# Kernel optimization log

Measured on AMD Instinct MI355X. Metric: run time of the kernel, lower is better.

## Reference

```python
import jax, jax.numpy as jnp
import numpy as np

N_NODES = 50000
N_EDGES = 1600000
IN_FEATS = 512
N_HIDDEN = 128
N_CLASSES = 40


def setup_inputs() -> dict:
    key = jax.random.key(0)
    k1, k2, k3, k4, k5, k6, k7 = jax.random.split(key, 7)
    features = jax.random.normal(k1, (N_NODES, IN_FEATS), dtype=jnp.float32)
    src = jax.random.randint(k2, (N_EDGES,), 0, N_NODES)
    dst = jax.random.randint(k3, (N_EDGES,), 0, N_NODES)
    # Glorot-ish init for weights, zeros for biases (DGL GraphConv defaults)
    W1 = jax.random.normal(k4, (IN_FEATS, N_HIDDEN), dtype=jnp.float32) / np.sqrt(IN_FEATS)
    b1 = jnp.zeros((N_HIDDEN,), dtype=jnp.float32)
    W2 = jax.random.normal(k5, (N_HIDDEN, N_CLASSES), dtype=jnp.float32) / np.sqrt(N_HIDDEN)
    b2 = jnp.zeros((N_CLASSES,), dtype=jnp.float32)
    return {"features": features, "W1": W1, "b1": b1, "W2": W2, "b2": b2,
            "src": src, "dst": dst}


def _norms(src, dst, n_nodes):
    ones = jnp.ones(src.shape[0], dtype=jnp.float32)
    deg_out = jax.ops.segment_sum(ones, src, num_segments=n_nodes)
    deg_in = jax.ops.segment_sum(ones, dst, num_segments=n_nodes)
    # clamp degree >= 1 as DGL does
    norm_src = jax.lax.rsqrt(jnp.maximum(deg_out, 1.0))
    norm_dst = jax.lax.rsqrt(jnp.maximum(deg_in, 1.0))
    return norm_src, norm_dst


def _graph_conv(x, W, b, src, dst, norm_src, norm_dst, n_nodes):
    # DGL GraphConv with norm='both'; in_feats > out_feats so W applied first
    h = x @ W                                   # [N, out]
    h = h * norm_src[:, None]                   # src-side D^{-1/2}
    msgs = h[src]                               # gather [E, out]
    agg = jax.ops.segment_sum(msgs, dst, num_segments=n_nodes)  # scatter-add
    agg = agg * norm_dst[:, None]               # dst-side D^{-1/2}
    return agg + b


def reference(features, W1, b1, W2, b2, src, dst):
    norm_src, norm_dst = _norms(src, dst, N_NODES)
    h = _graph_conv(features, W1, b1, src, dst, norm_src, norm_dst, N_NODES)
    h = jax.nn.relu(h)
    # dropout is identity at inference
    h = _graph_conv(h, W2, b2, src, dst, norm_src, norm_dst, N_NODES)
    return h
```

## Files before the change

kernel.cpp:

```cpp
#include <hip/hip_runtime.h>
#include <hip/hip_bf16.h>

#define N_NODES 50000
#define N_EDGES 1600000
#define IN_FEATS 512
#define N_HIDDEN 128
#define N_CLASSES 40
#define NBKT 782
#define NBLK 800
#define EPB 2000
#define NROWPAD 50048

typedef __attribute__((ext_vector_type(8))) short bf16x8;
typedef __attribute__((ext_vector_type(4))) float f32x4;

__device__ __forceinline__ unsigned short f2bf(float f) {
    unsigned u = __float_as_uint(f);
    u = (u + 0x7FFFu + ((u >> 16) & 1u)) >> 16;
    return (unsigned short)u;
}
__device__ __forceinline__ float bf2f(unsigned short h) {
    return __uint_as_float(((unsigned)h) << 16);
}
__device__ __forceinline__ unsigned pk_bf(float a, float b) {
    __hip_bfloat162 h = __float22bfloat162_rn(make_float2(a, b));
    union { __hip_bfloat162 v; unsigned u; } c;
    c.v = h;
    return c.u;
}

__device__ __forceinline__ void cvt8(float4 a, float4 b, bf16x8& h, bf16x8& l) {
    unsigned h0 = pk_bf(a.x, a.y), h1 = pk_bf(a.z, a.w);
    unsigned h2 = pk_bf(b.x, b.y), h3 = pk_bf(b.z, b.w);
    unsigned l0 = pk_bf(a.x - __uint_as_float(h0 << 16),
                        a.y - __uint_as_float(h0 & 0xffff0000u));
    unsigned l1 = pk_bf(a.z - __uint_as_float(h1 << 16),
                        a.w - __uint_as_float(h1 & 0xffff0000u));
    unsigned l2 = pk_bf(b.x - __uint_as_float(h2 << 16),
                        b.y - __uint_as_float(h2 & 0xffff0000u));
    unsigned l3 = pk_bf(b.z - __uint_as_float(h3 << 16),
                        b.w - __uint_as_float(h3 & 0xffff0000u));
    union U { unsigned u[4]; bf16x8 v; };
    U H; H.u[0] = h0; H.u[1] = h1; H.u[2] = h2; H.u[3] = h3; h = H.v;
    U L; L.u[0] = l0; L.u[1] = l1; L.u[2] = l2; L.u[3] = l3; l = L.v;
}

__global__ __launch_bounds__(256) void setup_cvt(
    const float* __restrict__ W1, const float* __restrict__ W2,
    unsigned short* __restrict__ W1ch, unsigned short* __restrict__ W1cl,
    unsigned short* __restrict__ W2th, unsigned short* __restrict__ W2tl) {
    int i = blockIdx.x * 256 + threadIdx.x;
    if (i < IN_FEATS * N_HIDDEN) {
        int k = i >> 7, c = i & 127;
        float v = W1[i];
        unsigned short h = f2bf(v);
        int o = (k >> 5) * 4096 + c * 32 + (k & 31);
        W1ch[o] = h;
        W1cl[o] = f2bf(v - bf2f(h));
    } else {
        int j = i - IN_FEATS * N_HIDDEN;
        int n = j >> 7, k = j & 127;
        float v = (n < N_CLASSES) ? W2[k * N_CLASSES + n] : 0.f;
        unsigned short h = f2bf(v);
        W2th[n * 128 + k] = h;
        W2tl[n * 128 + k] = f2bf(v - bf2f(h));
    }
}


#define MFJ(AH, AL, BH, BL, ACC)                                              \
    ACC = __builtin_amdgcn_mfma_f32_16x16x32_bf16(AH, BH, ACC, 0, 0, 0);      \
    ACC = __builtin_amdgcn_mfma_f32_16x16x32_bf16(AH, BL, ACC, 0, 0, 0);      \
    ACC = __builtin_amdgcn_mfma_f32_16x16x32_bf16(AL, BH, ACC, 0, 0, 0);

#define LOADB(KC)                                                             \
    const bf16x8 bh0 = *(const bf16x8*)(wbh + (KC) * 4096);                   \
    const bf16x8 bh1 = *(const bf16x8*)(wbh + (KC) * 4096 + 512);             \
    const bf16x8 bl0 = *(const bf16x8*)(wbl + (KC) * 4096);                   \
    const bf16x8 bl1 = *(const bf16x8*)(wbl + (KC) * 4096 + 512);

#define CORE()                                                                \
    bf16x8 ah0, al0, ah1, al1, ah2, al2, ah3, al3;                            \
    cvt8(xa00, xa01, ah0, al0); cvt8(xa10, xa11, ah1, al1);                   \
    cvt8(xa20, xa21, ah2, al2); cvt8(xa30, xa31, ah3, al3);                   \
    MFJ(ah0, al0, bh0, bl0, acc[0][0]) MFJ(ah0, al0, bh1, bl1, acc[0][1])     \
    MFJ(ah1, al1, bh0, bl0, acc[1][0]) MFJ(ah1, al1, bh1, bl1, acc[1][1])     \
    MFJ(ah2, al2, bh0, bl0, acc[2][0]) MFJ(ah2, al2, bh1, bl1, acc[2][1])     \
    MFJ(ah3, al3, bh0, bl0, acc[3][0]) MFJ(ah3, al3, bh1, bl1, acc[3][1])

__device__ __forceinline__ int imin(int a, int b) { return a < b ? a : b; }

__global__ __launch_bounds__(256) void megaA(
    const int* __restrict__ src, const int* __restrict__ dst,
    int* __restrict__ histD, int* __restrict__ histS,
    const float* __restrict__ X, const unsigned short* __restrict__ Wch,
    const unsigned short* __restrict__ Wcl, unsigned short* __restrict__ Hb) {
    __shared__ int hd[NBKT], hs[NBKT];
    const int tid = threadIdx.x;

    if (blockIdx.x >= NBKT) {
        int b = blockIdx.x - NBKT;
        for (int i = tid; i < NBKT; i += 256) { hd[i] = 0; hs[i] = 0; }
        __syncthreads();
        int e0 = b * EPB;
        for (int i = tid; i < EPB; i += 256) {
            atomicAdd(&hd[dst[e0 + i] >> 6], 1);
            atomicAdd(&hs[src[e0 + i] >> 6], 1);
        }
        __syncthreads();
        for (int i = tid; i < NBKT; i += 256) {
            histD[b * NBKT + i] = hd[i];
            histS[b * NBKT + i] = hs[i];
        }
        return;
    }
    const int lane = tid & 63;
    const int wv = tid >> 6;
    const int m = lane & 15;
    const int q = lane >> 4;
    const int q8 = q * 8;
    const int row0 = blockIdx.x * 64;

    const unsigned short* wbh = Wch + (wv * 32 + m) * 32 + q8;
    const unsigned short* wbl = Wcl + (wv * 32 + m) * 32 + q8;

    const float* xr0 = &X[(size_t)imin(row0 + m,      N_NODES - 1) * IN_FEATS + q8];
    const float* xr1 = &X[(size_t)imin(row0 + 16 + m, N_NODES - 1) * IN_FEATS + q8];
    const float* xr2 = &X[(size_t)imin(row0 + 32 + m, N_NODES - 1) * IN_FEATS + q8];
    const float* xr3 = &X[(size_t)imin(row0 + 48 + m, N_NODES - 1) * IN_FEATS + q8];

    f32x4 acc[4][2];
#pragma unroll
    for (int i = 0; i < 4; i++)
#pragma unroll
        for (int j = 0; j < 2; j++) acc[i][j] = (f32x4){0.f, 0.f, 0.f, 0.f};

    float4 xa00 = *(const float4*)(xr0),     xa01 = *(const float4*)(xr0 + 4);
    float4 xa10 = *(const float4*)(xr1),     xa11 = *(const float4*)(xr1 + 4);
    float4 xa20 = *(const float4*)(xr2),     xa21 = *(const float4*)(xr2 + 4);
    float4 xa30 = *(const float4*)(xr3),     xa31 = *(const float4*)(xr3 + 4);

    for (int kc = 0; kc < 15; kc++) {
        LOADB(kc)
        const int o = (kc + 1) * 32;
        float4 xn00 = *(const float4*)(xr0 + o), xn01 = *(const float4*)(xr0 + o + 4);
        float4 xn10 = *(const float4*)(xr1 + o), xn11 = *(const float4*)(xr1 + o + 4);
        float4 xn20 = *(const float4*)(xr2 + o), xn21 = *(const float4*)(xr2 + o + 4);
        float4 xn30 = *(const float4*)(xr3 + o), xn31 = *(const float4*)(xr3 + o + 4);
        CORE()
        xa00 = xn00; xa01 = xn01; xa10 = xn10; xa11 = xn11;
        xa20 = xn20; xa21 = xn21; xa30 = xn30; xa31 = xn31;
    }
    {
        LOADB(15)
        CORE()
    }

#pragma unroll
    for (int i = 0; i < 4; i++) {
#pragma unroll
        for (int r = 0; r < 4; r++) {
            int grow = row0 + i * 16 + q * 4 + r;
            if (grow < N_NODES) {
#pragma unroll
                for (int j = 0; j < 2; j++)
                    Hb[(size_t)grow * N_HIDDEN + wv * 32 + j * 16 + m] = f2bf(acc[i][j][r]);
            }
        }
    }
}

__global__ __launch_bounds__(256) void p2_local(
    const int* __restrict__ histD, const int* __restrict__ histS,
    int* __restrict__ baseD, int* __restrict__ baseS,
    int* __restrict__ totD, int* __restrict__ totS) {
    int wv = threadIdx.x >> 6, lane = threadIdx.x & 63;
    int w = blockIdx.x * 4 + wv;
    if (w >= NBKT) return;
    int runD = 0, runS = 0;
#pragma unroll
    for (int c = 0; c < 13; c++) {
        int blk = c * 64 + lane;
        int vD = 0, vS = 0;
        if (blk < NBLK) {
            vD = histD[blk * NBKT + w];
            vS = histS[blk * NBKT + w];
        }
        int iD = vD, iS = vS;
#pragma unroll
        for (int off = 1; off < 64; off <<= 1) {
            int tD = __shfl_up(iD, off);
            int tS = __shfl_up(iS, off);
            if (lane >= off) { iD += tD; iS += tS; }
        }
        if (blk < NBLK) {
            baseD[blk * NBKT + w] = runD + iD - vD;
            baseS[blk * NBKT + w] = runS + iS - vS;
        }
        runD += __shfl(iD, 63);
        runS += __shfl(iS, 63);
    }
    if (lane == 0) { totD[w] = runD; totS[w] = runS; }
}

__global__ __launch_bounds__(1024) void p2_small(
    const int* __restrict__ totD, const int* __restrict__ totS,
    int* __restrict__ bucket_base, int* __restrict__ srcb_base,
    int* __restrict__ offsets) {
    __shared__ int part[1024];
    int t = threadIdx.x;
    int v = (t < NBKT) ? totD[t] : 0;
    part[t] = v;
    __syncthreads();
    for (int off = 1; off < 1024; off <<= 1) {
        int x = (t >= off) ? part[t - off] : 0;
        __syncthreads();
        part[t] += x;
        __syncthreads();
    }
    if (t < NBKT) bucket_base[t] = part[t] - v;
    if (t == 0) { bucket_base[NBKT] = N_EDGES; offsets[N_NODES] = N_EDGES; }
    __syncthreads();
    v = (t < NBKT) ? totS[t] : 0;
    part[t] = v;
    __syncthreads();
    for (int off = 1; off < 1024; off <<= 1) {
        int x = (t >= off) ? part[t - off] : 0;
        __syncthreads();
        part[t] += x;
        __syncthreads();
    }
    if (t < NBKT) srcb_base[t] = part[t] - v;
    if (t == 0) srcb_base[NBKT] = N_EDGES;
}

__global__ __launch_bounds__(256) void p3_scatter(
    const int* __restrict__ src, const int* __restrict__ dst,
    const int* __restrict__ baseD, const int* __restrict__ baseS,
    const int* __restrict__ bucket_base, const int* __restrict__ srcb_base,
    unsigned int* __restrict__ edata, unsigned char* __restrict__ srcv) {
    __shared__ int curD[NBKT], curS[NBKT];
    int t = threadIdx.x, b = blockIdx.x;
    for (int i = t; i < NBKT; i += 256) {
        curD[i] = bucket_base[i] + baseD[b * NBKT + i];
        curS[i] = srcb_base[i] + baseS[b * NBKT + i];
    }
    __syncthreads();
    int e0 = b * EPB;
    for (int i = t; i < EPB; i += 256) {
        int s = src[e0 + i], d = dst[e0 + i];
        int slotD = atomicAdd(&curD[d >> 6], 1);
        edata[slotD] = (unsigned)s | ((unsigned)(d & 63) << 16);
        int slotS = atomicAdd(&curS[s >> 6], 1);
        srcv[slotS] = (unsigned char)(s & 63);
    }
}

__global__ __launch_bounds__(256) void p4_fused(
    const int* __restrict__ srcb_base, const unsigned char* __restrict__ srcv,
    const int* __restrict__ bucket_base, const unsigned int* __restrict__ edata,
    int* __restrict__ offsets, float* __restrict__ norm_src,
    float* __restrict__ norm_dst, int* __restrict__ sorted_src) {
    __shared__ int cntS[64], cntD[64], cur[64];
    int t = threadIdx.x, b = blockIdx.x;
    if (t < 64) { cntS[t] = 0; cntD[t] = 0; }
    __syncthreads();
    int s0 = srcb_base[b], s1 = srcb_base[b + 1];
    for (int i = s0 + t; i < s1; i += 256) atomicAdd(&cntS[srcv[i]], 1);
    int d0 = bucket_base[b], d1 = bucket_base[b + 1];
    for (int i = d0 + t; i < d1; i += 256)
        atomicAdd(&cntD[(edata[i] >> 16) & 63], 1);
    __syncthreads();
    if (t == 0) {
        int run = 0;
        for (int i = 0; i < 64; i++) { cur[i] = run; run += cntD[i]; }
    }
    __syncthreads();
    if (t < 64) {
        int node = b * 64 + t;
        if (node < N_NODES) {
            norm_src[node] = rsqrtf(fmaxf((float)cntS[t], 1.0f));
            offsets[node] = d0 + cur[t];
            norm_dst[node] = rsqrtf(fmaxf((float)cntD[t], 1.0f));
        }
    }
    __syncthreads();
    for (int i = d0 + t; i < d1; i += 256) {
        unsigned e = edata[i];
        int slot = atomicAdd(&cur[(e >> 16) & 63], 1);
        sorted_src[d0 + slot] = (int)(e & 0xFFFFu);
    }
}

#define FMA8(W, NS)                                                   \
    acc0 = fmaf(__uint_as_float((W).x << 16), NS, acc0);              \
    acc1 = fmaf(__uint_as_float((W).x & 0xffff0000u), NS, acc1);      \
    acc2 = fmaf(__uint_as_float((W).y << 16), NS, acc2);              \
    acc3 = fmaf(__uint_as_float((W).y & 0xffff0000u), NS, acc3);      \
    acc4 = fmaf(__uint_as_float((W).z << 16), NS, acc4);              \
    acc5 = fmaf(__uint_as_float((W).z & 0xffff0000u), NS, acc5);      \
    acc6 = fmaf(__uint_as_float((W).w << 16), NS, acc6);              \
    acc7 = fmaf(__uint_as_float((W).w & 0xffff0000u), NS, acc7);

__global__ __launch_bounds__(256) void agg1_kernel(
    const int* __restrict__ offsets, const int* __restrict__ sorted_src,
    const unsigned short* __restrict__ Hb, const float* __restrict__ norm_dst,
    const float* __restrict__ norm_src, const float* __restrict__ b1,
    unsigned short* __restrict__ H1h, unsigned short* __restrict__ H1l) {
    int wid = (blockIdx.x * 256 + threadIdx.x) >> 6;
    int lane = threadIdx.x & 63;
    if (wid >= N_NODES) return;
    int start = offsets[wid], end = offsets[wid + 1];
    int quad = lane >> 4;
    int c8 = (lane & 15) * 8;
    float acc0 = 0.f, acc1 = 0.f, acc2 = 0.f, acc3 = 0.f;
    float acc4 = 0.f, acc5 = 0.f, acc6 = 0.f, acc7 = 0.f;
    int base = start;
    for (; base + 16 <= end; base += 16) {
        int e0 = sorted_src[base + quad];
        int e1 = sorted_src[base + 4 + quad];
        int e2 = sorted_src[base + 8 + quad];
        int e3 = sorted_src[base + 12 + quad];
        float n0 = norm_src[e0], n1 = norm_src[e1];
        float n2 = norm_src[e2], n3 = norm_src[e3];
        uint4 w0 = *(const uint4*)&Hb[(size_t)e0 * N_HIDDEN + c8];
        uint4 w1 = *(const uint4*)&Hb[(size_t)e1 * N_HIDDEN + c8];
        uint4 w2 = *(const uint4*)&Hb[(size_t)e2 * N_HIDDEN + c8];
        uint4 w3 = *(const uint4*)&Hb[(size_t)e3 * N_HIDDEN + c8];
        FMA8(w0, n0);
        FMA8(w1, n1);
        FMA8(w2, n2);
        FMA8(w3, n3);
    }
    for (; base + 4 <= end; base += 4) {
        int e = sorted_src[base + quad];
        float n = norm_src[e];
        uint4 w = *(const uint4*)&Hb[(size_t)e * N_HIDDEN + c8];
        FMA8(w, n);
    }
    int rem = end - base;
    if (quad < rem) {
        int e = sorted_src[base + quad];
        float n = norm_src[e];
        uint4 w = *(const uint4*)&Hb[(size_t)e * N_HIDDEN + c8];
        FMA8(w, n);
    }
    acc0 += __shfl_xor(acc0, 16); acc0 += __shfl_xor(acc0, 32);
    acc1 += __shfl_xor(acc1, 16); acc1 += __shfl_xor(acc1, 32);
    acc2 += __shfl_xor(acc2, 16); acc2 += __shfl_xor(acc2, 32);
    acc3 += __shfl_xor(acc3, 16); acc3 += __shfl_xor(acc3, 32);
    acc4 += __shfl_xor(acc4, 16); acc4 += __shfl_xor(acc4, 32);
    acc5 += __shfl_xor(acc5, 16); acc5 += __shfl_xor(acc5, 32);
    acc6 += __shfl_xor(acc6, 16); acc6 += __shfl_xor(acc6, 32);
    acc7 += __shfl_xor(acc7, 16); acc7 += __shfl_xor(acc7, 32);
    if (quad == 0) {
        float nd = norm_dst[wid];
        float ns = norm_src[wid];
        float4 ba = *(const float4*)&b1[c8];
        float4 bb = *(const float4*)&b1[c8 + 4];
        float o[8];
        o[0] = fmaxf(acc0 * nd + ba.x, 0.f) * ns;
        o[1] = fmaxf(acc1 * nd + ba.y, 0.f) * ns;
        o[2] = fmaxf(acc2 * nd + ba.z, 0.f) * ns;
        o[3] = fmaxf(acc3 * nd + ba.w, 0.f) * ns;
        o[4] = fmaxf(acc4 * nd + bb.x, 0.f) * ns;
        o[5] = fmaxf(acc5 * nd + bb.y, 0.f) * ns;
        o[6] = fmaxf(acc6 * nd + bb.z, 0.f) * ns;
        o[7] = fmaxf(acc7 * nd + bb.w, 0.f) * ns;
        unsigned short hh[8], ll[8];
#pragma unroll
        for (int t = 0; t < 8; t++) {
            hh[t] = f2bf(o[t]);
            ll[t] = f2bf(o[t] - bf2f(hh[t]));
        }
        uint4 ph = make_uint4((unsigned)hh[0] | ((unsigned)hh[1] << 16),
                              (unsigned)hh[2] | ((unsigned)hh[3] << 16),
                              (unsigned)hh[4] | ((unsigned)hh[5] << 16),
                              (unsigned)hh[6] | ((unsigned)hh[7] << 16));
        uint4 pl = make_uint4((unsigned)ll[0] | ((unsigned)ll[1] << 16),
                              (unsigned)ll[2] | ((unsigned)ll[3] << 16),
                              (unsigned)ll[4] | ((unsigned)ll[5] << 16),
                              (unsigned)ll[6] | ((unsigned)ll[7] << 16));
        *(uint4*)&H1h[(size_t)wid * N_HIDDEN + c8] = ph;
        *(uint4*)&H1l[(size_t)wid * N_HIDDEN + c8] = pl;
    }
}

__global__ __launch_bounds__(256) void gemm2_kernel(
    const unsigned short* __restrict__ H1h, const unsigned short* __restrict__ H1l,
    const unsigned short* __restrict__ W2th, const unsigned short* __restrict__ W2tl,
    float* __restrict__ H2p) {
    __shared__ __align__(16) unsigned short Bh[48][136];
    __shared__ __align__(16) unsigned short Bl[48][136];
    const int tid = threadIdx.x;
    for (int i = tid; i < 48 * 16; i += 256) {
        int n = i >> 4, kq = (i & 15) * 8;
        *(uint4*)&Bh[n][kq] = *(const uint4*)&W2th[n * 128 + kq];
        *(uint4*)&Bl[n][kq] = *(const uint4*)&W2tl[n * 128 + kq];
    }
    __syncthreads();
    const int lane = tid & 63;
    const int wave = tid >> 6;
    const int m = lane & 15;
    const int q = lane >> 4;
    const int row0 = blockIdx.x * 128 + wave * 32;

    f32x4 acc[2][3];
#pragma unroll
    for (int i = 0; i < 2; i++)
#pragma unroll
        for (int j = 0; j < 3; j++) acc[i][j] = (f32x4){0.f, 0.f, 0.f, 0.f};

#pragma unroll
    for (int kc = 0; kc < 4; kc++) {
        bf16x8 bh[3], bl[3];
#pragma unroll
        for (int j = 0; j < 3; j++) {
            bh[j] = *(const bf16x8*)&Bh[j * 16 + m][kc * 32 + q * 8];
            bl[j] = *(const bf16x8*)&Bl[j * 16 + m][kc * 32 + q * 8];
        }
#pragma unroll
        for (int i = 0; i < 2; i++) {
            size_t ro = (size_t)(row0 + i * 16 + m) * N_HIDDEN + kc * 32 + q * 8;
            bf16x8 ah = *(const bf16x8*)&H1h[ro];
            bf16x8 al = *(const bf16x8*)&H1l[ro];
#pragma unroll
            for (int j = 0; j < 3; j++) {
                acc[i][j] = __builtin_amdgcn_mfma_f32_16x16x32_bf16(ah, bh[j], acc[i][j], 0, 0, 0);
                acc[i][j] = __builtin_amdgcn_mfma_f32_16x16x32_bf16(ah, bl[j], acc[i][j], 0, 0, 0);
                acc[i][j] = __builtin_amdgcn_mfma_f32_16x16x32_bf16(al, bh[j], acc[i][j], 0, 0, 0);
            }
        }
    }
#pragma unroll
    for (int i = 0; i < 2; i++) {
#pragma unroll
        for (int r = 0; r < 4; r++) {
            int row = row0 + i * 16 + q * 4 + r;
            if (row < N_NODES) {
#pragma unroll
                for (int j = 0; j < 3; j++) {
                    int col = j * 16 + m;
                    if (col < N_CLASSES)
                        H2p[(size_t)row * 64 + col] = acc[i][j][r];
                }
            }
        }
    }
}

__global__ __launch_bounds__(256) void agg2_kernel(
    const int* __restrict__ offsets, const int* __restrict__ sorted_src,
    const float* __restrict__ H2p, const float* __restrict__ norm_dst,
    const float* __restrict__ b2, float* __restrict__ OUT) {
    int wid = (blockIdx.x * 256 + threadIdx.x) >> 6;
    int lane = threadIdx.x & 63;
    if (wid >= N_NODES) return;
    int start = offsets[wid], end = offsets[wid + 1];
    int quad = lane >> 4;
    int c4 = (lane & 15) * 4;
    bool active = c4 < N_CLASSES;
    float4 acc = make_float4(0.f, 0.f, 0.f, 0.f);
    int base = start;
    for (; base + 16 <= end; base += 16) {
        int e0 = sorted_src[base + quad];
        int e1 = sorted_src[base + 4 + quad];
        int e2 = sorted_src[base + 8 + quad];
        int e3 = sorted_src[base + 12 + quad];
        if (active) {
            float4 v0 = *(const float4*)&H2p[(size_t)e0 * 64 + c4];
            float4 v1 = *(const float4*)&H2p[(size_t)e1 * 64 + c4];
            float4 v2 = *(const float4*)&H2p[(size_t)e2 * 64 + c4];
            float4 v3 = *(const float4*)&H2p[(size_t)e3 * 64 + c4];
            acc.x += (v0.x + v1.x) + (v2.x + v3.x);
            acc.y += (v0.y + v1.y) + (v2.y + v3.y);
            acc.z += (v0.z + v1.z) + (v2.z + v3.z);
            acc.w += (v0.w + v1.w) + (v2.w + v3.w);
        }
    }
    for (; base + 4 <= end; base += 4) {
        int e = sorted_src[base + quad];
        if (active) {
            float4 v = *(const float4*)&H2p[(size_t)e * 64 + c4];
            acc.x += v.x; acc.y += v.y; acc.z += v.z; acc.w += v.w;
        }
    }
    int rem = end - base;
    if (quad < rem && active) {
        int e = sorted_src[base + quad];
        float4 v = *(const float4*)&H2p[(size_t)e * 64 + c4];
        acc.x += v.x; acc.y += v.y; acc.z += v.z; acc.w += v.w;
    }
    acc.x += __shfl_xor(acc.x, 16); acc.x += __shfl_xor(acc.x, 32);
    acc.y += __shfl_xor(acc.y, 16); acc.y += __shfl_xor(acc.y, 32);
    acc.z += __shfl_xor(acc.z, 16); acc.z += __shfl_xor(acc.z, 32);
    acc.w += __shfl_xor(acc.w, 16); acc.w += __shfl_xor(acc.w, 32);
    if (lane < 10) {
        float nd = norm_dst[wid];
        float4 b = *(const float4*)&b2[lane * 4];
        acc.x = acc.x * nd + b.x;
        acc.y = acc.y * nd + b.y;
        acc.z = acc.z * nd + b.z;
        acc.w = acc.w * nd + b.w;
        *(float4*)&OUT[(size_t)wid * N_CLASSES + lane * 4] = acc;
    }
}

extern "C" void kernel_launch(void* const* d_in, const int* in_sizes, int n_in,
                              void* d_out, int out_size, void* d_ws, size_t ws_size,
                              hipStream_t stream) {
    const float* X   = (const float*)d_in[0];
    const float* W1  = (const float*)d_in[1];
    const float* b1  = (const float*)d_in[2];
    const float* W2  = (const float*)d_in[3];
    const float* b2  = (const float*)d_in[4];
    const int*   src = (const int*)d_in[5];
    const int*   dst = (const int*)d_in[6];
    float* out = (float*)d_out;

    float* norm_src   = (float*)d_ws;
    float* norm_dst   = norm_src + N_NODES;
    int*   offsets    = (int*)(norm_dst + N_NODES);
    int*   bucket_base = offsets + N_NODES + 16;
    int*   srcb_base  = bucket_base + 800;
    unsigned int* edata = (unsigned int*)(srcb_base + 800);
    unsigned char* srcv = (unsigned char*)(edata + N_EDGES);
    int*   sorted_src = (int*)(edata + N_EDGES) + 400000;
    int*   regionA    = sorted_src + N_EDGES;
    int*   histD      = regionA;
    int*   histS      = regionA + 625600;
    int*   baseD      = regionA + 1251200;
    int*   baseS      = regionA + 1876800;
    int*   totD       = regionA + 2502400;
    int*   totS       = regionA + 2503200;
    float* H2p        = (float*)regionA;
    unsigned short* H1h = (unsigned short*)(regionA + 3200000);
    unsigned short* H1l = H1h + (size_t)NROWPAD * N_HIDDEN;
    unsigned short* W1ch = H1l + (size_t)NROWPAD * N_HIDDEN;
    unsigned short* W1cl = W1ch + IN_FEATS * N_HIDDEN;
    unsigned short* W2th = W1cl + IN_FEATS * N_HIDDEN;
    unsigned short* W2tl = W2th + 48 * 128;
    unsigned short* Hb   = W2tl + 48 * 128;

    setup_cvt<<<(IN_FEATS * N_HIDDEN + 48 * 128) / 256, 256, 0, stream>>>(
        W1, W2, W1ch, W1cl, W2th, W2tl);
    megaA<<<NBLK + NBKT, 256, 0, stream>>>(src, dst, histD, histS, X, W1ch, W1cl, Hb);
    p2_local<<<(NBKT + 3) / 4, 256, 0, stream>>>(histD, histS, baseD, baseS, totD, totS);
    p2_small<<<1, 1024, 0, stream>>>(totD, totS, bucket_base, srcb_base, offsets);
    p3_scatter<<<NBLK, 256, 0, stream>>>(src, dst, baseD, baseS, bucket_base, srcb_base,
                                         edata, srcv);
    p4_fused<<<NBKT, 256, 0, stream>>>(srcb_base, srcv, bucket_base, edata,
                                       offsets, norm_src, norm_dst, sorted_src);
    agg1_kernel<<<(N_NODES + 3) / 4, 256, 0, stream>>>(offsets, sorted_src, Hb, norm_dst,
                                                       norm_src, b1, H1h, H1l);
    gemm2_kernel<<<(N_NODES + 127) / 128, 256, 0, stream>>>(H1h, H1l, W2th, W2tl, H2p);
    agg2_kernel<<<(N_NODES + 3) / 4, 256, 0, stream>>>(offsets, sorted_src, H2p, norm_dst, b2, out);
}
```

Measured before the change: 389.3 us.

## Share X tile via LDS double-buffer so each wave converts only its slice

Before, every wave in a block loaded and split into bf16 hi/lo all 64 rows of X for each K chunk, so the same conversion ran four times per block. Now each thread loads and converts one 8-element piece into a double-buffered LDS tile, and all waves read the shared hi/lo fragments from LDS. Global loads are prefetched two chunks ahead. This adds a __syncthreads per K step and LDS traffic in exchange for fewer redundant global loads and conversions.

```diff
diff --git a/kernel.cpp b/kernel.cpp
--- a/kernel.cpp
+++ b/kernel.cpp
@@ -44,6 +44,8 @@
     U H; H.u[0] = h0; H.u[1] = h1; H.u[2] = h2; H.u[3] = h3; h = H.v;
     U L; L.u[0] = l0; L.u[1] = l1; L.u[2] = l2; L.u[3] = l3; l = L.v;
 }
+
+__device__ __forceinline__ int imin(int a, int b) { return a < b ? a : b; }
 
 __global__ __launch_bounds__(256) void setup_cvt(
     const float* __restrict__ W1, const float* __restrict__ W2,
@@ -73,32 +75,17 @@
     ACC = __builtin_amdgcn_mfma_f32_16x16x32_bf16(AH, BL, ACC, 0, 0, 0);      \
     ACC = __builtin_amdgcn_mfma_f32_16x16x32_bf16(AL, BH, ACC, 0, 0, 0);
 
-#define LOADB(KC)                                                             \
-    const bf16x8 bh0 = *(const bf16x8*)(wbh + (KC) * 4096);                   \
-    const bf16x8 bh1 = *(const bf16x8*)(wbh + (KC) * 4096 + 512);             \
-    const bf16x8 bl0 = *(const bf16x8*)(wbl + (KC) * 4096);                   \
-    const bf16x8 bl1 = *(const bf16x8*)(wbl + (KC) * 4096 + 512);
-
-#define CORE()                                                                \
-    bf16x8 ah0, al0, ah1, al1, ah2, al2, ah3, al3;                            \
-    cvt8(xa00, xa01, ah0, al0); cvt8(xa10, xa11, ah1, al1);                   \
-    cvt8(xa20, xa21, ah2, al2); cvt8(xa30, xa31, ah3, al3);                   \
-    MFJ(ah0, al0, bh0, bl0, acc[0][0]) MFJ(ah0, al0, bh1, bl1, acc[0][1])     \
-    MFJ(ah1, al1, bh0, bl0, acc[1][0]) MFJ(ah1, al1, bh1, bl1, acc[1][1])     \
-    MFJ(ah2, al2, bh0, bl0, acc[2][0]) MFJ(ah2, al2, bh1, bl1, acc[2][1])     \
-    MFJ(ah3, al3, bh0, bl0, acc[3][0]) MFJ(ah3, al3, bh1, bl1, acc[3][1])
-
-__device__ __forceinline__ int imin(int a, int b) { return a < b ? a : b; }
-
 __global__ __launch_bounds__(256) void megaA(
     const int* __restrict__ src, const int* __restrict__ dst,
     int* __restrict__ histD, int* __restrict__ histS,
     const float* __restrict__ X, const unsigned short* __restrict__ Wch,
     const unsigned short* __restrict__ Wcl, unsigned short* __restrict__ Hb) {
-    __shared__ int hd[NBKT], hs[NBKT];
+    __shared__ __align__(16) unsigned char smem[16384];
     const int tid = threadIdx.x;
 
     if (blockIdx.x >= NBKT) {
+        int* hd = (int*)smem;
+        int* hs = hd + NBKT;
         int b = blockIdx.x - NBKT;
         for (int i = tid; i < NBKT; i += 256) { hd[i] = 0; hs[i] = 0; }
         __syncthreads();
@@ -114,6 +101,9 @@
         }
         return;
     }
+    typedef unsigned short ush;
+    ush* lds = (ush*)smem;
+
     const int lane = tid & 63;
     const int wv = tid >> 6;
     const int m = lane & 15;
@@ -124,10 +114,9 @@
     const unsigned short* wbh = Wch + (wv * 32 + m) * 32 + q8;
     const unsigned short* wbl = Wcl + (wv * 32 + m) * 32 + q8;
 
-    const float* xr0 = &X[(size_t)imin(row0 + m,      N_NODES - 1) * IN_FEATS + q8];
-    const float* xr1 = &X[(size_t)imin(row0 + 16 + m, N_NODES - 1) * IN_FEATS + q8];
-    const float* xr2 = &X[(size_t)imin(row0 + 32 + m, N_NODES - 1) * IN_FEATS + q8];
-    const float* xr3 = &X[(size_t)imin(row0 + 48 + m, N_NODES - 1) * IN_FEATS + q8];
+    const int srow = (tid >> 6) * 16 + (tid & 15);
+    const int sq8  = ((tid >> 4) & 3) * 8;
+    const float* xp = &X[(size_t)imin(row0 + srow, N_NODES - 1) * IN_FEATS + sq8];
 
     f32x4 acc[4][2];
 #pragma unroll
@@ -135,25 +124,52 @@
 #pragma unroll
         for (int j = 0; j < 2; j++) acc[i][j] = (f32x4){0.f, 0.f, 0.f, 0.f};
 
-    float4 xa00 = *(const float4*)(xr0),     xa01 = *(const float4*)(xr0 + 4);
-    float4 xa10 = *(const float4*)(xr1),     xa11 = *(const float4*)(xr1 + 4);
-    float4 xa20 = *(const float4*)(xr2),     xa21 = *(const float4*)(xr2 + 4);
-    float4 xa30 = *(const float4*)(xr3),     xa31 = *(const float4*)(xr3 + 4);
-
-    for (int kc = 0; kc < 15; kc++) {
-        LOADB(kc)
-        const int o = (kc + 1) * 32;
-        float4 xn00 = *(const float4*)(xr0 + o), xn01 = *(const float4*)(xr0 + o + 4);
-        float4 xn10 = *(const float4*)(xr1 + o), xn11 = *(const float4*)(xr1 + o + 4);
-        float4 xn20 = *(const float4*)(xr2 + o), xn21 = *(const float4*)(xr2 + o + 4);
-        float4 xn30 = *(const float4*)(xr3 + o), xn31 = *(const float4*)(xr3 + o + 4);
-        CORE()
-        xa00 = xn00; xa01 = xn01; xa10 = xn10; xa11 = xn11;
-        xa20 = xn20; xa21 = xn21; xa30 = xn30; xa31 = xn31;
-    }
     {
-        LOADB(15)
-        CORE()
+        float4 p0 = *(const float4*)(xp);
+        float4 p1 = *(const float4*)(xp + 4);
+        bf16x8 h, l;
+        cvt8(p0, p1, h, l);
+        *(bf16x8*)(lds + tid * 8) = h;
+        *(bf16x8*)(lds + 2048 + tid * 8) = l;
+    }
+    float4 a0 = *(const float4*)(xp + 32), a1 = *(const float4*)(xp + 36);
+    float4 b0 = *(const float4*)(xp + 64), b1 = *(const float4*)(xp + 68);
+    float4 n0 = a0, n1 = a1;
+    __syncthreads();
+
+    for (int kc = 0; kc < 16; kc++) {
+        const bf16x8 bh0 = *(const bf16x8*)(wbh + kc * 4096);
+        const bf16x8 bh1 = *(const bf16x8*)(wbh + kc * 4096 + 512);
+        const bf16x8 bl0 = *(const bf16x8*)(wbl + kc * 4096);
+        const bf16x8 bl1 = *(const bf16x8*)(wbl + kc * 4096 + 512);
+        if (kc < 13) {
+            n0 = *(const float4*)(xp + (kc + 3) * 32);
+            n1 = *(const float4*)(xp + (kc + 3) * 32 + 4);
+        }
+        if (kc < 15) {
+            ush* bufw = lds + ((kc + 1) & 1) * 4096;
+            bf16x8 h, l;
+            cvt8(a0, a1, h, l);
+            *(bf16x8*)(bufw + tid * 8) = h;
+            *(bf16x8*)(bufw + 2048 + tid * 8) = l;
+        }
+        const ush* bufr = lds + (kc & 1) * 4096;
+        bf16x8 ah0 = *(const bf16x8*)(bufr + (0 * 64 + lane) * 8);
+        bf16x8 ah1 = *(const bf16x8*)(bufr + (1 * 64 + lane) * 8);
+        bf16x8 ah2 = *(const bf16x8*)(bufr + (2 * 64 + lane) * 8);
+        bf16x8 ah3 = *(const bf16x8*)(bufr + (3 * 64 + lane) * 8);
+        bf16x8 al0 = *(const bf16x8*)(bufr + 2048 + (0 * 64 + lane) * 8);
+        bf16x8 al1 = *(const bf16x8*)(bufr + 2048 + (1 * 64 + lane) * 8);
+        bf16x8 al2 = *(const bf16x8*)(bufr + 2048 + (2 * 64 + lane) * 8);
+        bf16x8 al3 = *(const bf16x8*)(bufr + 2048 + (3 * 64 + lane) * 8);
+
+        MFJ(ah0, al0, bh0, bl0, acc[0][0]) MFJ(ah0, al0, bh1, bl1, acc[0][1])
+        MFJ(ah1, al1, bh0, bl0, acc[1][0]) MFJ(ah1, al1, bh1, bl1, acc[1][1])
+        MFJ(ah2, al2, bh0, bl0, acc[2][0]) MFJ(ah2, al2, bh1, bl1, acc[2][1])
+        MFJ(ah3, al3, bh0, bl0, acc[3][0]) MFJ(ah3, al3, bh1, bl1, acc[3][1])
+
+        if (kc < 15) __syncthreads();
+        a0 = b0; a1 = b1; b0 = n0; b1 = n1;
     }
 
 #pragma unroll
```

New measurement: 367.4 us. -5.6%, faster.
